# Kernel optimization log

Hardware: AMD Instinct MI355X
Metric: run time of the kernel (lower is better)

Reference implementation:

```python
import jax, jax.numpy as jnp
import numpy as np

BN_EPS = 1e-5


def conv1x1(x, w, b):
    # x: [B,C,H,W], w: [O,C], b: [O]
    return jnp.einsum('oc,bchw->bohw', w, x) + b[None, :, None, None]


def setup_inputs() -> dict:
    key = jax.random.key(0)
    ks = jax.random.split(key, 8)
    B, C, H, W = 4, 256, 64, 64
    Ci = C // 2  # inter_channels
    std = 0.01
    return {
        'x': jax.random.normal(ks[0], (B, C, H, W), dtype=jnp.float32),
        'w_g': jax.random.normal(ks[1], (Ci, C), dtype=jnp.float32) * std,
        'b_g': jnp.zeros((Ci,), jnp.float32),
        'w_theta': jax.random.normal(ks[2], (Ci, C), dtype=jnp.float32) * std,
        'b_theta': jnp.zeros((Ci,), jnp.float32),
        'w_phi': jax.random.normal(ks[3], (Ci, C), dtype=jnp.float32) * std,
        'b_phi': jnp.zeros((Ci,), jnp.float32),
        'w_out': jax.random.normal(ks[4], (C, Ci), dtype=jnp.float32) * std,
        'b_out': jnp.zeros((C,), jnp.float32),
        'bn_gamma': jax.random.normal(ks[5], (C,), dtype=jnp.float32),
        'bn_beta': jnp.zeros((C,), jnp.float32),
    }


def reference(x, w_g, b_g, w_theta, b_theta, w_phi, b_phi, w_out, b_out, bn_gamma, bn_beta):
    B, C, H, W = x.shape
    Ci = w_g.shape[0]
    N = H * W
    # 1x1 conv projections -> flatten spatial to tokens
    g_x = conv1x1(x, w_g, b_g).reshape(B, Ci, N)          # [B,Ci,N]
    theta_x = conv1x1(x, w_theta, b_theta).reshape(B, Ci, N)
    phi_x = conv1x1(x, w_phi, b_phi).reshape(B, Ci, N)
    # dense non-causal attention over N=HW tokens (no scaling)
    f = jnp.einsum('bcn,bcm->bnm', theta_x, phi_x)        # [B,N,N]
    f_div_C = jax.nn.softmax(f, axis=-1)
    y = jnp.einsum('bnm,bcm->bcn', f_div_C, g_x)          # [B,Ci,N]
    y = y.reshape(B, Ci, H, W)
    # output 1x1 conv + BatchNorm2d (training mode: batch statistics)
    W_y = conv1x1(y, w_out, b_out)                        # [B,C,H,W]
    mean = W_y.mean(axis=(0, 2, 3))
    var = W_y.var(axis=(0, 2, 3))
    W_y = (W_y - mean[None, :, None, None]) * jax.lax.rsqrt(var + BN_EPS)[None, :, None, None]
    W_y = W_y * bn_gamma[None, :, None, None] + bn_beta[None, :, None, None]
    return W_y + x
```

## Files before the change

### kernel.cpp

```cpp
#include <hip/hip_runtime.h>

#define N_TOK 4096
#define C_IN 256
#define CI_ 128

typedef unsigned short u16;
typedef unsigned int   u32;
typedef __attribute__((ext_vector_type(8))) short bf16x8;
typedef __attribute__((ext_vector_type(4))) float f32x4;

__device__ __forceinline__ float lo16f(u32 u){ union{u32 i; float f;} c; c.i = u << 16; return c.f; }
__device__ __forceinline__ float hi16f(u32 u){ union{u32 i; float f;} c; c.i = u & 0xffff0000u; return c.f; }
__device__ __forceinline__ void bf8f(const uint4 u, float* f){
    f[0]=lo16f(u.x); f[1]=hi16f(u.x); f[2]=lo16f(u.y); f[3]=hi16f(u.y);
    f[4]=lo16f(u.z); f[5]=hi16f(u.z); f[6]=lo16f(u.w); f[7]=hi16f(u.w);
}
__device__ __forceinline__ float bf1f(u16 v){ union{u32 i; float f;} c; c.i = ((u32)v)<<16; return c.f; }
__device__ __forceinline__ u16 f2bf(float f){
    union{float f; u32 i;} c; c.f = f;
    u32 i = c.i;
    u32 r = (i + 0x7fffu + ((i >> 16) & 1u)) >> 16;
    return (u16)r;
}
__device__ __forceinline__ u32 packbf(float a, float b){
    return (u32)f2bf(a) | ((u32)f2bf(b) << 16);
}

__device__ __forceinline__ void load8(const void* base, size_t idx, int flag, float* f){
    if (flag) {
        const float* p = (const float*)base + idx;
        *(float4*)&f[0] = *(const float4*)p;
        *(float4*)&f[4] = *(const float4*)(p + 4);
    } else {
        uint4 u = *(const uint4*)((const u16*)base + idx);
        bf8f(u, f);
    }
}
__device__ __forceinline__ void load4(const void* base, size_t idx, int flag, float* f){
    if (flag) {
        float4 v = *(const float4*)((const float*)base + idx);
        f[0]=v.x; f[1]=v.y; f[2]=v.z; f[3]=v.w;
    } else {
        uint2 u = *(const uint2*)((const u16*)base + idx);
        f[0]=lo16f(u.x); f[1]=hi16f(u.x); f[2]=lo16f(u.y); f[3]=hi16f(u.y);
    }
}

__device__ __forceinline__ void dma16(const u16* g, char* l){
    __builtin_amdgcn_global_load_lds(
        (const __attribute__((address_space(1))) u32*)g,
        (__attribute__((address_space(3))) u32*)l, 16, 0, 0);
}

__global__ __launch_bounds__(256) void convert_params_kernel(
    const void* wg, const void* wt, const void* wp, const void* wo,
    const void* bg, const void* bt, const void* bp, const void* bo,
    const void* gm, const void* bt2,
    int* __restrict__ flagp, float* __restrict__ canon, u16* __restrict__ canon_bf,
    float* __restrict__ stats)
{
    __shared__ int sflag;
    const int tid = threadIdx.x;
    if (tid < 64) {
        int cnt = 0;
        const u16* wgp = (const u16*)wg;
        for (int i = tid; i < 256; i += 64) {
            u16 v = wgp[2 * i];
            if (((v >> 7) & 0xFF) >= 128) cnt++;
        }
        #pragma unroll
        for (int off = 32; off; off >>= 1) cnt += __shfl_down(cnt, off);
        if (tid == 0) sflag = (cnt >= 8) ? 1 : 0;
    }
    __syncthreads();
    const int f = sflag;
    if (blockIdx.x == 0 && tid == 0) *flagp = f;

    int idx = blockIdx.x * 256 + tid;
    if (idx >= 132224) {
        int j = idx - 132224;
        if (j < 4096) stats[j] = 0.f;
        return;
    }
    const void* src; int loc;
    if      (idx < 32768)  { src = wg;  loc = idx; }
    else if (idx < 65536)  { src = wt;  loc = idx - 32768; }
    else if (idx < 98304)  { src = wp;  loc = idx - 65536; }
    else if (idx < 131072) { src = wo;  loc = idx - 98304; }
    else if (idx < 131200) { src = bg;  loc = idx - 131072; }
    else if (idx < 131328) { src = bt;  loc = idx - 131200; }
    else if (idx < 131456) { src = bp;  loc = idx - 131328; }
    else if (idx < 131712) { src = bo;  loc = idx - 131456; }
    else if (idx < 131968) { src = gm;  loc = idx - 131712; }
    else                   { src = bt2; loc = idx - 131968; }
    float v = f ? ((const float*)src)[loc] : bf1f(((const u16*)src)[loc]);
    canon[idx] = v;
    if (idx < 131072) canon_bf[idx] = f2bf(v);
}

__global__ __launch_bounds__(256) void xpose_kernel(
    const void* __restrict__ x, const int* __restrict__ flagp, u16* __restrict__ xbfT)
{
    __shared__ u16 t[64][72];
    const int flag = *flagp;
    const int b = blockIdx.z, k0 = blockIdx.y * 64, n0 = blockIdx.x * 64;
    const int tid = threadIdx.x;
    const size_t xb = (size_t)b * C_IN * N_TOK;
    {
        int kk = tid >> 4, n4 = (tid & 15) * 4;
        #pragma unroll
        for (int i = 0; i < 4; ++i) {
            float f[4];
            load4(x, xb + (size_t)(k0 + kk + i * 16) * N_TOK + n0 + n4, flag, f);
            #pragma unroll
            for (int j = 0; j < 4; ++j) t[n4 + j][kk + i * 16] = f2bf(f[j]);
        }
    }
    __syncthreads();
    {
        int kq = tid & 3, n = tid >> 2;
        u16* dst = &xbfT[((size_t)b * N_TOK + n0 + n) * C_IN + k0 + kq * 16];
        *(uint4*)(dst + 0) = *(const uint4*)&t[n][kq * 16];
        *(uint4*)(dst + 8) = *(const uint4*)&t[n][kq * 16 + 8];
    }
}

__global__ __launch_bounds__(512) void proj_kernel(
    const u16* __restrict__ xbfT, const float* __restrict__ canon,
    const u16* __restrict__ wbf,
    u16* __restrict__ gbuf, u16* __restrict__ tbufT, u16* __restrict__ pbufT)
{
    __shared__ __align__(16) u16 plds[64 * 400];
    const int b  = blockIdx.y;
    const int n0 = blockIdx.x * 64;
    const int tid = threadIdx.x;
    const int w    = tid >> 6;
    const int lane = tid & 63;
    const int col  = lane & 15;
    const int quad = lane >> 4;
    const int rw   = w * 48;
    const size_t bN = (size_t)b * N_TOK;

    f32x4 acc[3][4];
    #pragma unroll
    for (int i = 0; i < 3; ++i)
        #pragma unroll
        for (int j = 0; j < 4; ++j) acc[i][j] = (f32x4){0.f,0.f,0.f,0.f};

    #pragma unroll
    for (int kc = 0; kc < 8; ++kc) {
        bf16x8 bfr[4];
        #pragma unroll
        for (int nf = 0; nf < 4; ++nf)
            bfr[nf] = *(const bf16x8*)&xbfT[(bN + n0 + nf * 16 + col) * C_IN + kc * 32 + quad * 8];
        #pragma unroll
        for (int rs = 0; rs < 3; ++rs) {
            bf16x8 afr = *(const bf16x8*)&wbf[(size_t)(rw + rs * 16 + col) * 256 + kc * 32 + quad * 8];
            #pragma unroll
            for (int nf = 0; nf < 4; ++nf)
                acc[rs][nf] = __builtin_amdgcn_mfma_f32_16x16x32_bf16(afr, bfr[nf], acc[rs][nf], 0, 0, 0);
        }
    }

    #pragma unroll
    for (int rs = 0; rs < 3; ++rs) {
        int r0 = rw + rs * 16 + quad * 4;
        float b0 = canon[131072 + r0 + 0];
        float b1 = canon[131072 + r0 + 1];
        float b2 = canon[131072 + r0 + 2];
        float b3 = canon[131072 + r0 + 3];
        #pragma unroll
        for (int nf = 0; nf < 4; ++nf) {
            int n = nf * 16 + col;
            uint2 pv;
            pv.x = packbf(acc[rs][nf][0] + b0, acc[rs][nf][1] + b1);
            pv.y = packbf(acc[rs][nf][2] + b2, acc[rs][nf][3] + b3);
            *(uint2*)&plds[n * 400 + r0] = pv;
        }
    }
    __syncthreads();

    {
        int r = tid & 127, nq = tid >> 7;
        u16 tmp[16];
        #pragma unroll
        for (int j = 0; j < 16; ++j) tmp[j] = plds[(nq * 16 + j) * 400 + r];
        u16* dst = &gbuf[((size_t)b * CI_ + r) * N_TOK + n0 + nq * 16];
        *(uint4*)(dst + 0) = *(uint4*)&tmp[0];
        *(uint4*)(dst + 8) = *(uint4*)&tmp[8];
    }
    {
        int n = tid & 63, part = tid >> 6;
        const u16* src = (part < 4) ? &plds[n * 400 + 128 + part * 32]
                                    : &plds[n * 400 + 256 + (part - 4) * 32];
        u16* dst = (part < 4) ? &tbufT[(bN + n0 + n) * CI_ + part * 32]
                              : &pbufT[(bN + n0 + n) * CI_ + (part - 4) * 32];
        #pragma unroll
        for (int v = 0; v < 4; ++v) *(uint4*)(dst + v * 8) = *(const uint4*)(src + v * 8);
    }
}

#define PB2   131072
#define MST2  147456
#define LST2  147712
#define SMEM2 147968

__global__ __launch_bounds__(512) void attn_kernel(
    const u16* __restrict__ tbufT, const u16* __restrict__ pbufT,
    const u16* __restrict__ gbuf,
    const u16* __restrict__ wbf, const float* __restrict__ canon,
    u16* __restrict__ wyb, float* __restrict__ stats)
{
    __shared__ __align__(16) char smem[SMEM2];
    const int b   = blockIdx.y;
    const int q0  = blockIdx.x * 64;
    const int tid = threadIdx.x;
    const int w    = tid >> 6;
    const int lane = tid & 63;
    const int col  = lane & 15;
    const int quad = lane >> 4;
    const int wq   = w & 3;
    const int ms   = w >> 2;
    const int qw   = wq * 16;
    const size_t bN = (size_t)b * N_TOK;
    const size_t bC = (size_t)b * CI_;

    bf16x8 thf[4];
    {
        const u16* tb = tbufT + (bN + q0 + qw + col) * CI_;
        #pragma unroll
        for (int kc = 0; kc < 4; ++kc)
            thf[kc] = *(const bf16x8*)(tb + kc * 32 + quad * 8);
    }

    const u16* sb[8];
    int ldso[8];
    int sstep;
    if (w < 4) {
        int r = lane >> 4, cp = lane & 15;
        sstep = 128 * CI_;
        #pragma unroll
        for (int j = 0; j < 8; ++j) {
            int seg = w * 8 + j, p = seg >> 4, m0 = (seg & 15) * 4;
            int m = m0 + r, h = cp ^ (m & 15);
            sb[j] = pbufT + (bN + p * 64 + m) * CI_ + h * 8;
            ldso[j] = p * 16384 + m0 * 256;
        }
    } else {
        int r = lane >> 3, cp = lane & 7;
        sstep = 128;
        #pragma unroll
        for (int j = 0; j < 8; ++j) {
            int seg = (w - 4) * 8 + j, p = seg >> 4, c0 = (seg & 15) * 8;
            int c = c0 + r, h = cp ^ (c & 7);
            sb[j] = gbuf + (bC + c) * N_TOK + p * 64 + h * 8;
            ldso[j] = 65536 + p * 16384 + c0 * 128;
        }
    }

    f32x4 yacc[8];
    #pragma unroll
    for (int i = 0; i < 8; ++i) yacc[i] = (f32x4){0.f, 0.f, 0.f, 0.f};
    float m_st = -3.0e38f, l_st = 0.f;

    #pragma unroll
    for (int j = 0; j < 8; ++j) dma16(sb[j], smem + ldso[j]);

    for (int s = 0; s < 32; ++s) {
        const int bb = (s & 1) << 15;
        __asm volatile("s_waitcnt lgkmcnt(0)" ::: "memory");
        __asm volatile("s_barrier" ::: "memory");
        if (s < 31) {
            const int nb = ((s + 1) & 1) << 15;
            const size_t so = (size_t)(s + 1) * sstep;
            #pragma unroll
            for (int j = 0; j < 8; ++j) dma16(sb[j] + so, smem + nb + ldso[j]);
            __asm volatile("s_waitcnt vmcnt(8)" ::: "memory");
        } else {
            __asm volatile("s_waitcnt vmcnt(0)" ::: "memory");
        }
        __asm volatile("s_barrier" ::: "memory");

        f32x4 sacc[4];
        #pragma unroll
        for (int i = 0; i < 4; ++i) sacc[i] = (f32x4){0.f, 0.f, 0.f, 0.f};
        #pragma unroll
        for (int kc = 0; kc < 4; ++kc) {
            #pragma unroll
            for (int msub = 0; msub < 4; ++msub) {
                int m = msub * 16 + col;
                int h = kc * 4 + quad;
                bf16x8 af = *(const bf16x8*)(smem + bb + ms * 16384 + m * 256 + ((h ^ (m & 15)) << 4));
                sacc[msub] = __builtin_amdgcn_mfma_f32_16x16x32_bf16(af, thf[kc], sacc[msub], 0, 0, 0);
            }
        }

        float tmax = sacc[0][0];
        #pragma unroll
        for (int i = 0; i < 4; ++i)
            #pragma unroll
            for (int r = 0; r < 4; ++r) tmax = fmaxf(tmax, sacc[i][r]);
        tmax = fmaxf(tmax, __shfl_xor(tmax, 16));
        tmax = fmaxf(tmax, __shfl_xor(tmax, 32));
        float m_new = fmaxf(m_st, tmax);
        float p16[16], ps = 0.f;
        #pragma unroll
        for (int i = 0; i < 4; ++i)
            #pragma unroll
            for (int r = 0; r < 4; ++r) {
                float pv = __expf(sacc[i][r] - m_new);
                p16[i * 4 + r] = pv;
                ps += pv;
            }
        ps += __shfl_xor(ps, 16);
        ps += __shfl_xor(ps, 32);
        float alpha = __expf(m_st - m_new);
        l_st = l_st * alpha + ps;
        m_st = m_new;
        #pragma unroll
        for (int i = 0; i < 8; ++i) {
            yacc[i][0] *= alpha; yacc[i][1] *= alpha;
            yacc[i][2] *= alpha; yacc[i][3] *= alpha;
        }

        {
            char* pb = smem + PB2 + w * 2048 + col * 128;
            #pragma unroll
            for (int msub = 0; msub < 4; ++msub) {
                #pragma unroll
                for (int pr = 0; pr < 2; ++pr) {
                    u32 d = packbf(p16[msub * 4 + pr * 2], p16[msub * 4 + pr * 2 + 1]);
                    int h = msub * 2 + (quad >> 1);
                    *(u32*)(pb + ((h ^ (col & 7)) << 4) + (quad & 1) * 8 + pr * 4) = d;
                }
            }
        }
        __asm volatile("s_waitcnt lgkmcnt(0)" ::: "memory");

        bf16x8 pf[2];
        #pragma unroll
        for (int km = 0; km < 2; ++km) {
            int h = km * 4 + quad;
            pf[km] = *(const bf16x8*)(smem + PB2 + w * 2048 + col * 128 + ((h ^ (col & 7)) << 4));
        }
        #pragma unroll
        for (int csub = 0; csub < 8; ++csub) {
            #pragma unroll
            for (int km = 0; km < 2; ++km) {
                int c = csub * 16 + col;
                int h = km * 4 + quad;
                bf16x8 gf = *(const bf16x8*)(smem + 65536 + bb + ms * 16384 + c * 128 + ((h ^ (c & 7)) << 4));
                yacc[csub] = __builtin_amdgcn_mfma_f32_16x16x32_bf16(gf, pf[km], yacc[csub], 0, 0, 0);
            }
        }
    }

    __syncthreads();
    if (ms == 1) {
        char* mb = smem + wq * 8192 + col * 512;
        #pragma unroll
        for (int csub = 0; csub < 8; ++csub)
            *(f32x4*)(mb + (((csub * 4 + quad) ^ col) << 4)) = yacc[csub];
        if (quad == 0) {
            *(float*)(smem + MST2 + (wq * 16 + col) * 4) = m_st;
            *(float*)(smem + LST2 + (wq * 16 + col) * 4) = l_st;
        }
    }
    __syncthreads();
    if (ms == 0) {
        float m1 = *(const float*)(smem + MST2 + (wq * 16 + col) * 4);
        float l1 = *(const float*)(smem + LST2 + (wq * 16 + col) * 4);
        float M  = fmaxf(m_st, m1);
        float a0 = __expf(m_st - M), a1 = __expf(m1 - M);
        float li = 1.f / (l_st * a0 + l1 * a1);
        float s0 = a0 * li, s1 = a1 * li;
        const char* mb = smem + wq * 8192 + col * 512;
        const int q = qw + col;
        #pragma unroll
        for (int csub = 0; csub < 8; ++csub) {
            f32x4 y1 = *(const f32x4*)(mb + (((csub * 4 + quad) ^ col) << 4));
            uint2 pv;
            pv.x = packbf(yacc[csub][0] * s0 + y1[0] * s1, yacc[csub][1] * s0 + y1[1] * s1);
            pv.y = packbf(yacc[csub][2] * s0 + y1[2] * s1, yacc[csub][3] * s0 + y1[3] * s1);
            int chunk = csub * 2 + (quad >> 1);
            *(uint2*)(smem + 32768 + q * 256 + ((chunk ^ (q & 15)) << 4) + (quad & 1) * 8) = pv;
        }
    }
    __syncthreads();

    const u16* wo = wbf + 98304;
    f32x4 oacc[2][4];
    #pragma unroll
    for (int i = 0; i < 2; ++i)
        #pragma unroll
        for (int j = 0; j < 4; ++j) oacc[i][j] = (f32x4){0.f,0.f,0.f,0.f};
    #pragma unroll
    for (int kc = 0; kc < 4; ++kc) {
        bf16x8 bqf[4];
        #pragma unroll
        for (int qf = 0; qf < 4; ++qf) {
            int q = qf * 16 + col;
            int h = kc * 4 + quad;
            bqf[qf] = *(const bf16x8*)(smem + 32768 + q * 256 + ((h ^ (q & 15)) << 4));
        }
        #pragma unroll
        for (int os = 0; os < 2; ++os) {
            bf16x8 afr = *(const bf16x8*)&wo[(size_t)(w * 32 + os * 16 + col) * CI_ + kc * 32 + quad * 8];
            #pragma unroll
            for (int qf = 0; qf < 4; ++qf)
                oacc[os][qf] = __builtin_amdgcn_mfma_f32_16x16x32_bf16(afr, bqf[qf], oacc[os][qf], 0, 0, 0);
        }
    }
    const int bucket = (blockIdx.x + blockIdx.y) & 7;
    float* sbk = stats + bucket * 512;
    #pragma unroll
    for (int os = 0; os < 2; ++os) {
        int ob = w * 32 + os * 16 + quad * 4;
        #pragma unroll
        for (int i = 0; i < 4; ++i) {
            float bb2 = canon[131456 + ob + i];
            float s1 = 0.f, s2 = 0.f;
            u16* dst = &wyb[((size_t)b * C_IN + ob + i) * N_TOK + q0 + col];
            #pragma unroll
            for (int qf = 0; qf < 4; ++qf) {
                float v = oacc[os][qf][i] + bb2;
                dst[qf * 16] = f2bf(v);
                s1 += v;
                s2 += v * v;
            }
            #pragma unroll
            for (int off = 8; off; off >>= 1) {
                s1 += __shfl_xor(s1, off);
                s2 += __shfl_xor(s2, off);
            }
            if (col == 0) {
                atomicAdd(&sbk[ob + i], s1);
                atomicAdd(&sbk[256 + ob + i], s2);
            }
        }
    }
}

__global__ __launch_bounds__(256) void bnorm_kernel(
    const u16* __restrict__ wyb, const void* __restrict__ x,
    const float* __restrict__ stats,
    const float* __restrict__ canon, const int* __restrict__ flagp,
    void* __restrict__ outv)
{
    const int flag = *flagp;
    size_t base = ((size_t)blockIdx.x * 256 + threadIdx.x) * 8;
    int o = (int)((base >> 12) & 255);
    float sum1 = 0.f, sum2 = 0.f;
    #pragma unroll
    for (int k = 0; k < 8; ++k) {
        sum1 += stats[k * 512 + o];
        sum2 += stats[k * 512 + 256 + o];
    }
    float mean = sum1 * (1.f / 16384.f);
    float var  = sum2 * (1.f / 16384.f) - mean * mean;
    float r = rsqrtf(var + 1e-5f);
    float gm = canon[131712 + o], bt = canon[131968 + o];
    uint4 wu = *(const uint4*)&wyb[base];
    float wv[8]; bf8f(wu, wv);
    float xf[8]; load8(x, base, flag, xf);
    float ov[8];
    #pragma unroll
    for (int i = 0; i < 8; ++i)
        ov[i] = (wv[i] - mean) * r * gm + bt + xf[i];
    if (flag) {
        float* op = (float*)outv + base;
        *(float4*)op       = *(float4*)&ov[0];
        *(float4*)(op + 4) = *(float4*)&ov[4];
    } else {
        uint4 res;
        res.x = packbf(ov[0], ov[1]);
        res.y = packbf(ov[2], ov[3]);
        res.z = packbf(ov[4], ov[5]);
        res.w = packbf(ov[6], ov[7]);
        *(uint4*)((u16*)outv + base) = res;
    }
}

extern "C" void kernel_launch(void* const* d_in, const int* in_sizes, int n_in,
                              void* d_out, int out_size, void* d_ws, size_t ws_size,
                              hipStream_t stream)
{
    const void* x   = d_in[0];
    const void* w_g = d_in[1];
    const void* b_g = d_in[2];
    const void* w_t = d_in[3];
    const void* b_t = d_in[4];
    const void* w_p = d_in[5];
    const void* b_p = d_in[6];
    const void* w_o = d_in[7];
    const void* b_o = d_in[8];
    const void* gm  = d_in[9];
    const void* bt  = d_in[10];

    char* base = (char*)d_ws;
    float* canon    = (float*)base;
    u16*   canon_bf = (u16*)(base + 528896);
    int*   flagp    = (int*)(base + 791040);
    float* stats    = (float*)(base + 791296);
    u16*   gbuf     = (u16*)(base + 1048576);
    u16*   tbufT    = (u16*)(base + 5242880);
    u16*   pbufT    = (u16*)(base + 9437184);
    u16*   wyb      = (u16*)(base + 13631488);
    u16*   xbfT     = (u16*)(base + 22020096);

    convert_params_kernel<<<533, 256, 0, stream>>>(w_g, w_t, w_p, w_o, b_g, b_t, b_p, b_o,
                                                   gm, bt, flagp, canon, canon_bf, stats);
    xpose_kernel<<<dim3(64, 4, 4), 256, 0, stream>>>(x, flagp, xbfT);
    proj_kernel<<<dim3(64, 4), 512, 0, stream>>>(xbfT, canon, canon_bf, gbuf, tbufT, pbufT);
    attn_kernel<<<dim3(64, 4), 512, 0, stream>>>(tbufT, pbufT, gbuf, canon_bf, canon, wyb, stats);
    bnorm_kernel<<<2048, 256, 0, stream>>>(wyb, x, stats, canon, flagp, d_out);
}
```

Before: 188.0 us.

## Split attention KV into halves with 128-query tiles, add merge kernel, fuse prep

The attention kernel now handles 128 queries per block, with two query fragments per wave sharing each K/V tile loaded into LDS. The key dimension is split into two halves across blockIdx.z, giving split-KV partial outputs plus (max, sum) that a new merge kernel combines before the output projection and BN stats. The parameter conversion and x transpose kernels are fused into a single prep launch. This doubles K/V reuse per LDS load while keeping the same block count, at the cost of more registers, an extra global round trip for partial results, and an additional kernel launch.

Measured after the change: 178.7 us. 1.05x faster.

```diff
diff --git a/kernel.cpp b/kernel.cpp
--- a/kernel.cpp
+++ b/kernel.cpp
@@ -52,14 +52,15 @@
         (__attribute__((address_space(3))) u32*)l, 16, 0, 0);
 }
 
-__global__ __launch_bounds__(256) void convert_params_kernel(
-    const void* wg, const void* wt, const void* wp, const void* wo,
+__global__ __launch_bounds__(256) void prep_kernel(
+    const void* x, const void* wg, const void* wt, const void* wp, const void* wo,
     const void* bg, const void* bt, const void* bp, const void* bo,
     const void* gm, const void* bt2,
     int* __restrict__ flagp, float* __restrict__ canon, u16* __restrict__ canon_bf,
-    float* __restrict__ stats)
+    float* __restrict__ stats, u16* __restrict__ xbfT)
 {
     __shared__ int sflag;
+    __shared__ u16 t[64][72];
     const int tid = threadIdx.x;
     if (tid < 64) {
         int cnt = 0;
@@ -73,55 +74,53 @@
         if (tid == 0) sflag = (cnt >= 8) ? 1 : 0;
     }
     __syncthreads();
-    const int f = sflag;
-    if (blockIdx.x == 0 && tid == 0) *flagp = f;
-
-    int idx = blockIdx.x * 256 + tid;
-    if (idx >= 132224) {
-        int j = idx - 132224;
-        if (j < 4096) stats[j] = 0.f;
-        return;
-    }
-    const void* src; int loc;
-    if      (idx < 32768)  { src = wg;  loc = idx; }
-    else if (idx < 65536)  { src = wt;  loc = idx - 32768; }
-    else if (idx < 98304)  { src = wp;  loc = idx - 65536; }
-    else if (idx < 131072) { src = wo;  loc = idx - 98304; }
-    else if (idx < 131200) { src = bg;  loc = idx - 131072; }
-    else if (idx < 131328) { src = bt;  loc = idx - 131200; }
-    else if (idx < 131456) { src = bp;  loc = idx - 131328; }
-    else if (idx < 131712) { src = bo;  loc = idx - 131456; }
-    else if (idx < 131968) { src = gm;  loc = idx - 131712; }
-    else                   { src = bt2; loc = idx - 131968; }
-    float v = f ? ((const float*)src)[loc] : bf1f(((const u16*)src)[loc]);
-    canon[idx] = v;
-    if (idx < 131072) canon_bf[idx] = f2bf(v);
-}
-
-__global__ __launch_bounds__(256) void xpose_kernel(
-    const void* __restrict__ x, const int* __restrict__ flagp, u16* __restrict__ xbfT)
-{
-    __shared__ u16 t[64][72];
-    const int flag = *flagp;
-    const int b = blockIdx.z, k0 = blockIdx.y * 64, n0 = blockIdx.x * 64;
-    const int tid = threadIdx.x;
-    const size_t xb = (size_t)b * C_IN * N_TOK;
-    {
-        int kk = tid >> 4, n4 = (tid & 15) * 4;
-        #pragma unroll
-        for (int i = 0; i < 4; ++i) {
-            float f[4];
-            load4(x, xb + (size_t)(k0 + kk + i * 16) * N_TOK + n0 + n4, flag, f);
-            #pragma unroll
-            for (int j = 0; j < 4; ++j) t[n4 + j][kk + i * 16] = f2bf(f[j]);
-        }
-    }
-    __syncthreads();
-    {
-        int kq = tid & 3, n = tid >> 2;
-        u16* dst = &xbfT[((size_t)b * N_TOK + n0 + n) * C_IN + k0 + kq * 16];
-        *(uint4*)(dst + 0) = *(const uint4*)&t[n][kq * 16];
-        *(uint4*)(dst + 8) = *(const uint4*)&t[n][kq * 16 + 8];
+    const int flag = sflag;
+    const int bid = blockIdx.x;
+
+    if (bid < 549) {
+        if (bid == 0 && tid == 0) *flagp = flag;
+        int idx = bid * 256 + tid;
+        if (idx >= 132224) {
+            int j = idx - 132224;
+            if (j < 4096) stats[j] = 0.f;
+            return;
+        }
+        const void* src; int loc;
+        if      (idx < 32768)  { src = wg;  loc = idx; }
+        else if (idx < 65536)  { src = wt;  loc = idx - 32768; }
+        else if (idx < 98304)  { src = wp;  loc = idx - 65536; }
+        else if (idx < 131072) { src = wo;  loc = idx - 98304; }
+        else if (idx < 131200) { src = bg;  loc = idx - 131072; }
+        else if (idx < 131328) { src = bt;  loc = idx - 131200; }
+        else if (idx < 131456) { src = bp;  loc = idx - 131328; }
+        else if (idx < 131712) { src = bo;  loc = idx - 131456; }
+        else if (idx < 131968) { src = gm;  loc = idx - 131712; }
+        else                   { src = bt2; loc = idx - 131968; }
+        float v = flag ? ((const float*)src)[loc] : bf1f(((const u16*)src)[loc]);
+        canon[idx] = v;
+        if (idx < 131072) canon_bf[idx] = f2bf(v);
+    } else {
+        int tb = bid - 549;
+        int nb = tb & 63, kb = (tb >> 6) & 3, b = tb >> 8;
+        const int k0 = kb * 64, n0 = nb * 64;
+        const size_t xb = (size_t)b * C_IN * N_TOK;
+        {
+            int kk = tid >> 4, n4 = (tid & 15) * 4;
+            #pragma unroll
+            for (int i = 0; i < 4; ++i) {
+                float f[4];
+                load4(x, xb + (size_t)(k0 + kk + i * 16) * N_TOK + n0 + n4, flag, f);
+                #pragma unroll
+                for (int j = 0; j < 4; ++j) t[n4 + j][kk + i * 16] = f2bf(f[j]);
+            }
+        }
+        __syncthreads();
+        {
+            int kq = tid & 3, n = tid >> 2;
+            u16* dst = &xbfT[((size_t)b * N_TOK + n0 + n) * C_IN + k0 + kq * 16];
+            *(uint4*)(dst + 0) = *(const uint4*)&t[n][kq * 16];
+            *(uint4*)(dst + 8) = *(const uint4*)&t[n][kq * 16 + 8];
+        }
     }
 }
 
@@ -200,20 +199,23 @@
     }
 }
 
-#define PB2   131072
-#define MST2  147456
-#define LST2  147712
-#define SMEM2 147968
+#define PH4   0
+#define G4    65536
+#define PB4   131072
+#define MST4  131072
+#define LST4  (131072 + 512)
+#define SMEM4 147456
 
 __global__ __launch_bounds__(512) void attn_kernel(
     const u16* __restrict__ tbufT, const u16* __restrict__ pbufT,
     const u16* __restrict__ gbuf,
-    const u16* __restrict__ wbf, const float* __restrict__ canon,
-    u16* __restrict__ wyb, float* __restrict__ stats)
+    u16* __restrict__ yp, float* __restrict__ ml)
 {
-    __shared__ __align__(16) char smem[SMEM2];
+    __shared__ __align__(16) char smem[SMEM4];
+    const int bx  = blockIdx.x;
     const int b   = blockIdx.y;
-    const int q0  = blockIdx.x * 64;
+    const int mh  = blockIdx.z;
+    const int q0  = bx * 128;
     const int tid = threadIdx.x;
     const int w    = tid >> 6;
     const int lane = tid & 63;
@@ -221,19 +223,20 @@
     const int quad = lane >> 4;
     const int wq   = w & 3;
     const int ms   = w >> 2;
-    const int qw   = wq * 16;
     const size_t bN = (size_t)b * N_TOK;
     const size_t bC = (size_t)b * CI_;
-
-    bf16x8 thf[4];
-    {
-        const u16* tb = tbufT + (bN + q0 + qw + col) * CI_;
+    const int mbase = mh * 2048;
+
+    bf16x8 thf[2][4];
+    #pragma unroll
+    for (int qf = 0; qf < 2; ++qf) {
+        const u16* tb = tbufT + (bN + q0 + wq * 32 + qf * 16 + col) * CI_;
         #pragma unroll
         for (int kc = 0; kc < 4; ++kc)
-            thf[kc] = *(const bf16x8*)(tb + kc * 32 + quad * 8);
-    }
-
-    const u16* sb[8];
+            thf[qf][kc] = *(const bf16x8*)(tb + kc * 32 + quad * 8);
+    }
+
+    const u16* sbp[8];
     int ldso[8];
     int sstep;
     if (w < 4) {
@@ -243,8 +246,8 @@
         for (int j = 0; j < 8; ++j) {
             int seg = w * 8 + j, p = seg >> 4, m0 = (seg & 15) * 4;
             int m = m0 + r, h = cp ^ (m & 15);
-            sb[j] = pbufT + (bN + p * 64 + m) * CI_ + h * 8;
-            ldso[j] = p * 16384 + m0 * 256;
+            sbp[j] = pbufT + (bN + mbase + p * 64 + m) * CI_ + h * 8;
+            ldso[j] = PH4 + p * 16384 + m0 * 256;
         }
     } else {
         int r = lane >> 3, cp = lane & 7;
@@ -253,141 +256,220 @@
         for (int j = 0; j < 8; ++j) {
             int seg = (w - 4) * 8 + j, p = seg >> 4, c0 = (seg & 15) * 8;
             int c = c0 + r, h = cp ^ (c & 7);
-            sb[j] = gbuf + (bC + c) * N_TOK + p * 64 + h * 8;
-            ldso[j] = 65536 + p * 16384 + c0 * 128;
-        }
-    }
-
-    f32x4 yacc[8];
-    #pragma unroll
-    for (int i = 0; i < 8; ++i) yacc[i] = (f32x4){0.f, 0.f, 0.f, 0.f};
-    float m_st = -3.0e38f, l_st = 0.f;
-
-    #pragma unroll
-    for (int j = 0; j < 8; ++j) dma16(sb[j], smem + ldso[j]);
-
-    for (int s = 0; s < 32; ++s) {
+            sbp[j] = gbuf + (bC + c) * N_TOK + mbase + p * 64 + h * 8;
+            ldso[j] = G4 + p * 16384 + c0 * 128;
+        }
+    }
+
+    f32x4 yacc[2][8];
+    #pragma unroll
+    for (int qf = 0; qf < 2; ++qf)
+        #pragma unroll
+        for (int i = 0; i < 8; ++i) yacc[qf][i] = (f32x4){0.f, 0.f, 0.f, 0.f};
+    float m_st[2] = {-3.0e38f, -3.0e38f};
+    float l_st[2] = {0.f, 0.f};
+
+    #pragma unroll
+    for (int j = 0; j < 8; ++j) dma16(sbp[j], smem + ldso[j]);
+
+    for (int s = 0; s < 16; ++s) {
         const int bb = (s & 1) << 15;
         __asm volatile("s_waitcnt lgkmcnt(0)" ::: "memory");
         __asm volatile("s_barrier" ::: "memory");
-        if (s < 31) {
+        if (s < 15) {
             const int nb = ((s + 1) & 1) << 15;
             const size_t so = (size_t)(s + 1) * sstep;
             #pragma unroll
-            for (int j = 0; j < 8; ++j) dma16(sb[j] + so, smem + nb + ldso[j]);
+            for (int j = 0; j < 8; ++j) dma16(sbp[j] + so, smem + nb + ldso[j]);
             __asm volatile("s_waitcnt vmcnt(8)" ::: "memory");
         } else {
             __asm volatile("s_waitcnt vmcnt(0)" ::: "memory");
         }
         __asm volatile("s_barrier" ::: "memory");
 
-        f32x4 sacc[4];
-        #pragma unroll
-        for (int i = 0; i < 4; ++i) sacc[i] = (f32x4){0.f, 0.f, 0.f, 0.f};
+        f32x4 sacc[4][2];
+        #pragma unroll
+        for (int i = 0; i < 4; ++i) {
+            sacc[i][0] = (f32x4){0.f, 0.f, 0.f, 0.f};
+            sacc[i][1] = (f32x4){0.f, 0.f, 0.f, 0.f};
+        }
         #pragma unroll
         for (int kc = 0; kc < 4; ++kc) {
             #pragma unroll
             for (int msub = 0; msub < 4; ++msub) {
                 int m = msub * 16 + col;
                 int h = kc * 4 + quad;
-                bf16x8 af = *(const bf16x8*)(smem + bb + ms * 16384 + m * 256 + ((h ^ (m & 15)) << 4));
-                sacc[msub] = __builtin_amdgcn_mfma_f32_16x16x32_bf16(af, thf[kc], sacc[msub], 0, 0, 0);
-            }
-        }
-
-        float tmax = sacc[0][0];
-        #pragma unroll
-        for (int i = 0; i < 4; ++i)
-            #pragma unroll
-            for (int r = 0; r < 4; ++r) tmax = fmaxf(tmax, sacc[i][r]);
-        tmax = fmaxf(tmax, __shfl_xor(tmax, 16));
-        tmax = fmaxf(tmax, __shfl_xor(tmax, 32));
-        float m_new = fmaxf(m_st, tmax);
-        float p16[16], ps = 0.f;
-        #pragma unroll
-        for (int i = 0; i < 4; ++i)
-            #pragma unroll
-            for (int r = 0; r < 4; ++r) {
-                float pv = __expf(sacc[i][r] - m_new);
-                p16[i * 4 + r] = pv;
-                ps += pv;
-            }
-        ps += __shfl_xor(ps, 16);
-        ps += __shfl_xor(ps, 32);
-        float alpha = __expf(m_st - m_new);
-        l_st = l_st * alpha + ps;
-        m_st = m_new;
-        #pragma unroll
-        for (int i = 0; i < 8; ++i) {
-            yacc[i][0] *= alpha; yacc[i][1] *= alpha;
-            yacc[i][2] *= alpha; yacc[i][3] *= alpha;
-        }
-
-        {
-            char* pb = smem + PB2 + w * 2048 + col * 128;
-            #pragma unroll
-            for (int msub = 0; msub < 4; ++msub) {
+                bf16x8 af = *(const bf16x8*)(smem + PH4 + bb + ms * 16384 + m * 256 + ((h ^ (m & 15)) << 4));
+                sacc[msub][0] = __builtin_amdgcn_mfma_f32_16x16x32_bf16(af, thf[0][kc], sacc[msub][0], 0, 0, 0);
+                sacc[msub][1] = __builtin_amdgcn_mfma_f32_16x16x32_bf16(af, thf[1][kc], sacc[msub][1], 0, 0, 0);
+            }
+        }
+
+        float pp[2][16];
+        #pragma unroll
+        for (int qf = 0; qf < 2; ++qf) {
+            float tmax = sacc[0][qf][0];
+            #pragma unroll
+            for (int i = 0; i < 4; ++i)
                 #pragma unroll
-                for (int pr = 0; pr < 2; ++pr) {
-                    u32 d = packbf(p16[msub * 4 + pr * 2], p16[msub * 4 + pr * 2 + 1]);
-                    int h = msub * 2 + (quad >> 1);
-                    *(u32*)(pb + ((h ^ (col & 7)) << 4) + (quad & 1) * 8 + pr * 4) = d;
+                for (int r = 0; r < 4; ++r) tmax = fmaxf(tmax, sacc[i][qf][r]);
+            tmax = fmaxf(tmax, __shfl_xor(tmax, 16));
+            tmax = fmaxf(tmax, __shfl_xor(tmax, 32));
+            float m_new = fmaxf(m_st[qf], tmax);
+            float ps = 0.f;
+            #pragma unroll
+            for (int i = 0; i < 4; ++i)
+                #pragma unroll
+                for (int r = 0; r < 4; ++r) {
+                    float pv = __expf(sacc[i][qf][r] - m_new);
+                    pp[qf][i * 4 + r] = pv;
+                    ps += pv;
                 }
-            }
-        }
-        __asm volatile("s_waitcnt lgkmcnt(0)" ::: "memory");
-
-        bf16x8 pf[2];
+            ps += __shfl_xor(ps, 16);
+            ps += __shfl_xor(ps, 32);
+            float alpha = __expf(m_st[qf] - m_new);
+            l_st[qf] = l_st[qf] * alpha + ps;
+            m_st[qf] = m_new;
+            #pragma unroll
+            for (int i = 0; i < 8; ++i) {
+                yacc[qf][i][0] *= alpha; yacc[qf][i][1] *= alpha;
+                yacc[qf][i][2] *= alpha; yacc[qf][i][3] *= alpha;
+            }
+        }
+
+        char* pb = smem + PB4 + w * 2048;
         #pragma unroll
         for (int km = 0; km < 2; ++km) {
-            int h = km * 4 + quad;
-            pf[km] = *(const bf16x8*)(smem + PB2 + w * 2048 + col * 128 + ((h ^ (col & 7)) << 4));
-        }
-        #pragma unroll
-        for (int csub = 0; csub < 8; ++csub) {
-            #pragma unroll
-            for (int km = 0; km < 2; ++km) {
+            __asm volatile("s_waitcnt lgkmcnt(0)" ::: "memory");
+            #pragma unroll
+            for (int qf = 0; qf < 2; ++qf) {
+                #pragma unroll
+                for (int mi = 0; mi < 2; ++mi) {
+                    int msub = km * 2 + mi;
+                    int hl = mi * 2 + (quad >> 1);
+                    #pragma unroll
+                    for (int pr = 0; pr < 2; ++pr) {
+                        u32 d = packbf(pp[qf][msub * 4 + pr * 2], pp[qf][msub * 4 + pr * 2 + 1]);
+                        *(u32*)(pb + qf * 1024 + col * 64 + ((hl ^ (col & 3)) << 4) + (quad & 1) * 8 + pr * 4) = d;
+                    }
+                }
+            }
+            __asm volatile("s_waitcnt lgkmcnt(0)" ::: "memory");
+            bf16x8 pf0 = *(const bf16x8*)(pb + 0    + col * 64 + ((quad ^ (col & 3)) << 4));
+            bf16x8 pf1 = *(const bf16x8*)(pb + 1024 + col * 64 + ((quad ^ (col & 3)) << 4));
+            #pragma unroll
+            for (int csub = 0; csub < 8; ++csub) {
                 int c = csub * 16 + col;
                 int h = km * 4 + quad;
-                bf16x8 gf = *(const bf16x8*)(smem + 65536 + bb + ms * 16384 + c * 128 + ((h ^ (c & 7)) << 4));
-                yacc[csub] = __builtin_amdgcn_mfma_f32_16x16x32_bf16(gf, pf[km], yacc[csub], 0, 0, 0);
+                bf16x8 gf = *(const bf16x8*)(smem + G4 + bb + ms * 16384 + c * 128 + ((h ^ (c & 7)) << 4));
+                yacc[0][csub] = __builtin_amdgcn_mfma_f32_16x16x32_bf16(gf, pf0, yacc[0][csub], 0, 0, 0);
+                yacc[1][csub] = __builtin_amdgcn_mfma_f32_16x16x32_bf16(gf, pf1, yacc[1][csub], 0, 0, 0);
             }
         }
     }
 
     __syncthreads();
+    const int mb0 = (wq < 2) ? wq * 16384 : 65536 + (wq - 2) * 16384;
     if (ms == 1) {
-        char* mb = smem + wq * 8192 + col * 512;
-        #pragma unroll
-        for (int csub = 0; csub < 8; ++csub)
-            *(f32x4*)(mb + (((csub * 4 + quad) ^ col) << 4)) = yacc[csub];
-        if (quad == 0) {
-            *(float*)(smem + MST2 + (wq * 16 + col) * 4) = m_st;
-            *(float*)(smem + LST2 + (wq * 16 + col) * 4) = l_st;
+        #pragma unroll
+        for (int qf = 0; qf < 2; ++qf) {
+            char* mb = smem + mb0 + qf * 8192 + col * 512;
+            #pragma unroll
+            for (int csub = 0; csub < 8; ++csub)
+                *(f32x4*)(mb + (((csub * 4 + quad) ^ col) << 4)) = yacc[qf][csub];
+            if (quad == 0) {
+                int idx = wq * 32 + qf * 16 + col;
+                *(float*)(smem + MST4 + idx * 4) = m_st[qf];
+                *(float*)(smem + LST4 + idx * 4) = l_st[qf];
+            }
         }
     }
     __syncthreads();
     if (ms == 0) {
-        float m1 = *(const float*)(smem + MST2 + (wq * 16 + col) * 4);
-        float l1 = *(const float*)(smem + LST2 + (wq * 16 + col) * 4);
-        float M  = fmaxf(m_st, m1);
-        float a0 = __expf(m_st - M), a1 = __expf(m1 - M);
-        float li = 1.f / (l_st * a0 + l1 * a1);
-        float s0 = a0 * li, s1 = a1 * li;
-        const char* mb = smem + wq * 8192 + col * 512;
-        const int q = qw + col;
-        #pragma unroll
-        for (int csub = 0; csub < 8; ++csub) {
-            f32x4 y1 = *(const f32x4*)(mb + (((csub * 4 + quad) ^ col) << 4));
-            uint2 pv;
-            pv.x = packbf(yacc[csub][0] * s0 + y1[0] * s1, yacc[csub][1] * s0 + y1[1] * s1);
-            pv.y = packbf(yacc[csub][2] * s0 + y1[2] * s1, yacc[csub][3] * s0 + y1[3] * s1);
-            int chunk = csub * 2 + (quad >> 1);
-            *(uint2*)(smem + 32768 + q * 256 + ((chunk ^ (q & 15)) << 4) + (quad & 1) * 8) = pv;
-        }
+        #pragma unroll
+        for (int qf = 0; qf < 2; ++qf) {
+            int idx = wq * 32 + qf * 16 + col;
+            float m1 = *(const float*)(smem + MST4 + idx * 4);
+            float l1 = *(const float*)(smem + LST4 + idx * 4);
+            float M  = fmaxf(m_st[qf], m1);
+            float a0 = __expf(m_st[qf] - M), a1 = __expf(m1 - M);
+            float lt = l_st[qf] * a0 + l1 * a1;
+            float li = 1.f / lt;
+            float s0 = a0 * li, s1 = a1 * li;
+            const char* mb = smem + mb0 + qf * 8192 + col * 512;
+            const int q = q0 + idx;
+            u16* yo = yp + ((size_t)(mh * 4 + b) * N_TOK + q) * CI_ + quad * 4;
+            #pragma unroll
+            for (int csub = 0; csub < 8; ++csub) {
+                f32x4 y1 = *(const f32x4*)(mb + (((csub * 4 + quad) ^ col) << 4));
+                uint2 pv;
+                pv.x = packbf(yacc[qf][csub][0] * s0 + y1[0] * s1,
+                              yacc[qf][csub][1] * s0 + y1[1] * s1);
+                pv.y = packbf(yacc[qf][csub][2] * s0 + y1[2] * s1,
+                              yacc[qf][csub][3] * s0 + y1[3] * s1);
+                *(uint2*)(yo + csub * 16) = pv;
+            }
+            if (quad == 0) {
+                float* mlp = ml + ((size_t)(mh * 4 + b) * N_TOK + q) * 2;
+                mlp[0] = M;
+                mlp[1] = lt;
+            }
+        }
+    }
+}
+
+__global__ __launch_bounds__(512) void merge_kernel(
+    const u16* __restrict__ yp, const float* __restrict__ ml,
+    const u16* __restrict__ wbf, const float* __restrict__ canon,
+    u16* __restrict__ wyb, float* __restrict__ stats)
+{
+    __shared__ __align__(16) char smem[16384];
+    __shared__ float sc[2][64];
+    const int bx = blockIdx.x;
+    const int b  = blockIdx.y;
+    const int n0 = bx * 64;
+    const int tid = threadIdx.x;
+
+    if (tid < 64) {
+        size_t q = (size_t)n0 + tid;
+        const float* p0 = ml + ((size_t)b * N_TOK + q) * 2;
+        const float* p1 = ml + ((size_t)(4 + b) * N_TOK + q) * 2;
+        float m0 = p0[0], l0 = p0[1];
+        float m1 = p1[0], l1 = p1[1];
+        float M = fmaxf(m0, m1);
+        float a0 = __expf(m0 - M) * l0;
+        float a1 = __expf(m1 - M) * l1;
+        float inv = 1.f / (a0 + a1);
+        sc[0][tid] = a0 * inv;
+        sc[1][tid] = a1 * inv;
     }
     __syncthreads();
-
+    {
+        int q = tid >> 3, c16 = (tid & 7) * 16;
+        const u16* p0 = yp + ((size_t)b * N_TOK + n0 + q) * CI_ + c16;
+        const u16* p1 = yp + ((size_t)(4 + b) * N_TOK + n0 + q) * CI_ + c16;
+        float s0 = sc[0][q], s1 = sc[1][q];
+        #pragma unroll
+        for (int c8 = 0; c8 < 2; ++c8) {
+            uint4 u0 = *(const uint4*)(p0 + c8 * 8);
+            uint4 u1 = *(const uint4*)(p1 + c8 * 8);
+            float f0[8], f1[8];
+            bf8f(u0, f0); bf8f(u1, f1);
+            uint4 res;
+            res.x = packbf(f0[0]*s0 + f1[0]*s1, f0[1]*s0 + f1[1]*s1);
+            res.y = packbf(f0[2]*s0 + f1[2]*s1, f0[3]*s0 + f1[3]*s1);
+            res.z = packbf(f0[4]*s0 + f1[4]*s1, f0[5]*s0 + f1[5]*s1);
+            res.w = packbf(f0[6]*s0 + f1[6]*s1, f0[7]*s0 + f1[7]*s1);
+            int chunk = (c16 >> 3) + c8;
+            *(uint4*)(smem + q * 256 + ((chunk ^ (q & 15)) << 4)) = res;
+        }
+    }
+    __syncthreads();
+
+    const int w    = tid >> 6;
+    const int lane = tid & 63;
+    const int col  = lane & 15;
+    const int quad = lane >> 4;
     const u16* wo = wbf + 98304;
     f32x4 oacc[2][4];
     #pragma unroll
@@ -401,7 +483,7 @@
         for (int qf = 0; qf < 4; ++qf) {
             int q = qf * 16 + col;
             int h = kc * 4 + quad;
-            bqf[qf] = *(const bf16x8*)(smem + 32768 + q * 256 + ((h ^ (q & 15)) << 4));
+            bqf[qf] = *(const bf16x8*)(smem + q * 256 + ((h ^ (q & 15)) << 4));
         }
         #pragma unroll
         for (int os = 0; os < 2; ++os) {
@@ -411,7 +493,7 @@
                 oacc[os][qf] = __builtin_amdgcn_mfma_f32_16x16x32_bf16(afr, bqf[qf], oacc[os][qf], 0, 0, 0);
         }
     }
-    const int bucket = (blockIdx.x + blockIdx.y) & 7;
+    const int bucket = (bx + b) & 7;
     float* sbk = stats + bucket * 512;
     #pragma unroll
     for (int os = 0; os < 2; ++os) {
@@ -420,7 +502,7 @@
         for (int i = 0; i < 4; ++i) {
             float bb2 = canon[131456 + ob + i];
             float s1 = 0.f, s2 = 0.f;
-            u16* dst = &wyb[((size_t)b * C_IN + ob + i) * N_TOK + q0 + col];
+            u16* dst = &wyb[((size_t)b * C_IN + ob + i) * N_TOK + n0 + col];
             #pragma unroll
             for (int qf = 0; qf < 4; ++qf) {
                 float v = oacc[os][qf][i] + bb2;
@@ -507,11 +589,13 @@
     u16*   pbufT    = (u16*)(base + 9437184);
     u16*   wyb      = (u16*)(base + 13631488);
     u16*   xbfT     = (u16*)(base + 22020096);
-
-    convert_params_kernel<<<533, 256, 0, stream>>>(w_g, w_t, w_p, w_o, b_g, b_t, b_p, b_o,
-                                                   gm, bt, flagp, canon, canon_bf, stats);
-    xpose_kernel<<<dim3(64, 4, 4), 256, 0, stream>>>(x, flagp, xbfT);
+    u16*   yp       = (u16*)(base + 30408704);
+    float* ml       = (float*)(base + 38797312);
+
+    prep_kernel<<<1573, 256, 0, stream>>>(x, w_g, w_t, w_p, w_o, b_g, b_t, b_p, b_o,
+                                          gm, bt, flagp, canon, canon_bf, stats, xbfT);
     proj_kernel<<<dim3(64, 4), 512, 0, stream>>>(xbfT, canon, canon_bf, gbuf, tbufT, pbufT);
-    attn_kernel<<<dim3(64, 4), 512, 0, stream>>>(tbufT, pbufT, gbuf, canon_bf, canon, wyb, stats);
+    attn_kernel<<<dim3(32, 4, 2), 512, 0, stream>>>(tbufT, pbufT, gbuf, yp, ml);
+    merge_kernel<<<dim3(64, 4), 512, 0, stream>>>(yp, ml, canon_bf, canon, wyb, stats);
     bnorm_kernel<<<2048, 256, 0, stream>>>(wyb, x, stats, canon, flagp, d_out);
 }
```
